# Performance work log

Hardware: AMD Instinct MI355X
Metric: run time of the kernel (lower is better)

## Reference

```python
import jax, jax.numpy as jnp
import numpy as np

B, S, D, H, F, V = 64, 64, 512, 8, 2048, 8192
L = 6
ENC_C = 2048  # InceptionV3 feature channels
NEG_INF = jnp.float32(-jnp.inf)


def _layernorm(x, g, b, eps=1e-3):
    mu = jnp.mean(x, axis=-1, keepdims=True)
    var = jnp.var(x, axis=-1, keepdims=True)
    return (x - mu) * jax.lax.rsqrt(var + eps) * g + b


def _mha(q_in, kv_in, Wq, Wk, Wv, Wo, causal=False):
    Bq, Sq, Dm = q_in.shape
    Sk = kv_in.shape[1]
    dh = Dm // H
    q = (q_in @ Wq).reshape(Bq, Sq, H, dh)
    k = (kv_in @ Wk).reshape(Bq, Sk, H, dh)
    v = (kv_in @ Wv).reshape(Bq, Sk, H, dh)
    scores = jnp.einsum('bqhd,bkhd->bhqk', q, k) / jnp.sqrt(jnp.float32(dh))
    if causal:
        mask = jnp.tril(jnp.ones((Sq, Sk), dtype=bool))
        scores = jnp.where(mask, scores, jnp.float32(-1e9))
    a = jax.nn.softmax(scores, axis=-1)
    o = jnp.einsum('bhqk,bkhd->bqhd', a, v).reshape(Bq, Sq, Dm)
    return o @ Wo


def replacement_mask(targets):
    # out[b,i,v] = -inf iff some j<=i has targets[b,j]==v and v!=0
    valid = (targets != 0)[..., None].astype(jnp.float32)  # (B,S,1)
    oh = jax.nn.one_hot(targets, V, dtype=jnp.float32) * valid  # (B,S,V)
    seen = jnp.cumsum(oh, axis=1) > 0
    return jnp.where(seen, NEG_INF, jnp.float32(0.0))


def setup_inputs() -> dict:
    key = jax.random.key(0)
    ks = jax.random.split(key, 32)
    n = lambda i, shp, sc=0.02: jax.random.normal(ks[i], shp, jnp.float32) * sc
    inp = {
        'enc_feat': jax.random.normal(ks[0], (B, 8, 8, ENC_C), jnp.float32),
        'targets': jax.random.randint(ks[1], (B, S), 0, V, jnp.int32),
        'conv_w': n(2, (ENC_C, D)), 'conv_b': jnp.zeros((D,), jnp.float32),
        'tok_emb': n(3, (V, D)), 'pos_emb': n(4, (S, D)),
        'Wq_s': n(5, (L, D, D)), 'Wk_s': n(6, (L, D, D)),
        'Wv_s': n(7, (L, D, D)), 'Wo_s': n(8, (L, D, D)),
        'Wq_c': n(9, (L, D, D)), 'Wk_c': n(10, (L, D, D)),
        'Wv_c': n(11, (L, D, D)), 'Wo_c': n(12, (L, D, D)),
        'W1': n(13, (L, D, F)), 'fb1': jnp.zeros((L, F), jnp.float32),
        'W2': n(14, (L, F, D)), 'fb2': jnp.zeros((L, D), jnp.float32),
        'g1': jnp.ones((L, D), jnp.float32), 'be1': jnp.zeros((L, D), jnp.float32),
        'g2': jnp.ones((L, D), jnp.float32), 'be2': jnp.zeros((L, D), jnp.float32),
        'g3': jnp.ones((L, D), jnp.float32), 'be3': jnp.zeros((L, D), jnp.float32),
        'Wout': n(15, (D, V)), 'bout': jnp.zeros((V,), jnp.float32),
    }
    return inp


def reference(enc_feat, conv_w, conv_b, tok_emb, pos_emb,
              Wq_s, Wk_s, Wv_s, Wo_s, Wq_c, Wk_c, Wv_c, Wo_c,
              W1, fb1, W2, fb2, g1, be1, g2, be2, g3, be3,
              Wout, bout, targets):
    # 1x1 conv == per-pixel matmul, then flatten spatial -> (B, 64, D)
    enc = enc_feat.reshape(B, -1, ENC_C) @ conv_w + conv_b
    # decoder: token + positional embedding
    x = tok_emb[targets] + pos_emb[None, :, :]
    for l in range(L):
        a1 = _mha(x, x, Wq_s[l], Wk_s[l], Wv_s[l], Wo_s[l], causal=True)
        x = _layernorm(x + a1, g1[l], be1[l])
        a2 = _mha(x, enc, Wq_c[l], Wk_c[l], Wv_c[l], Wo_c[l])
        x = _layernorm(x + a2, g2[l], be2[l])
        ff = jax.nn.relu(x @ W1[l] + fb1[l]) @ W2[l] + fb2[l]
        x = _layernorm(x + ff, g3[l], be3[l])
    logits = x @ Wout + bout
    return logits + replacement_mask(targets)
```

## Files before the change

kernel.cpp:

```cpp
#include <hip/hip_runtime.h>
#include <cstdint>
#include <cstddef>

#define SS   64
#define BB   64
#define DM   512
#define NH   8
#define DH   64
#define FF   2048
#define VV   8192
#define LL   6
#define ENCC 2048
#define MR   4096

#define MASK_SENTINEL -3.0e38f

typedef unsigned short u16;
typedef __attribute__((ext_vector_type(8))) short bf16x8;
typedef __attribute__((ext_vector_type(4))) float f32x4;

__device__ __forceinline__ u16 f2b(float f) {
    union { float f; uint32_t u; } c; c.f = f;
    uint32_t u = c.u;
    return (u16)((u + 0x7fffu + ((u >> 16) & 1u)) >> 16);
}
__device__ __forceinline__ float blo(uint32_t p) {
    union { uint32_t u; float f; } c; c.u = p << 16; return c.f;
}
__device__ __forceinline__ float bhi(uint32_t p) {
    union { uint32_t u; float f; } c; c.u = p & 0xffff0000u; return c.f;
}

#define GLL(g, l) __builtin_amdgcn_global_load_lds( \
    (const __attribute__((address_space(1))) void*)(g), \
    (__attribute__((address_space(3))) void*)(l), 16, 0, 0)

template<int BMT>
__global__ __launch_bounds__(256) void gemm_bf16(
    const u16* __restrict__ A, const u16* __restrict__ BT,
    const float* __restrict__ bias, u16* __restrict__ Cb,
    int K, int ldc, int relu, int nsplit,
    const u16* __restrict__ A2, const u16* __restrict__ BT2,
    u16* __restrict__ C2, int ldc2)
{
    constexpr int WM = BMT / 2;
    constexpr int AI = WM / 16;
    constexpr int TILE = (BMT + 128) * 32;
    __shared__ __align__(16) u16 smem[2 * TILE];
    const int tid = threadIdx.x;
    const int wave = tid >> 6, lane = tid & 63;

    int bx = blockIdx.x;
    const u16* Ab = A; const u16* Bb = BT; u16* Cp = Cb; int ld = ldc;
    const float* bi = bias; int rl = relu;
    if (bx >= nsplit) { bx -= nsplit; Ab = A2; Bb = BT2; Cp = C2; ld = ldc2; bi = nullptr; rl = 0; }

    const int m0 = blockIdx.y * BMT, n0 = bx * 128;
    const int srow = wave * 16 + (lane >> 2);
    const int scol = (lane & 3) * 8;
    const u16* Ap  = Ab + (size_t)(m0 + srow) * K + scol;
    const u16* Bp  = Bb + (size_t)(n0 + srow) * K + scol;
    const u16* Ap2 = Ap + (size_t)64 * K;
    const u16* Bp2 = Bp + (size_t)64 * K;
    const int aW = wave * 16 * 32;
    const int bW = BMT * 32 + wave * 16 * 32;

    const int wm = wave >> 1, wn = wave & 1;
    const int q = lane >> 4, mr = lane & 15;
    const int aRd = (wm * WM + mr) * 32 + q * 8;
    const int bRd = BMT * 32 + (wn * 64 + mr) * 32 + q * 8;

    f32x4 acc[AI][4];
    const f32x4 z = {0.f, 0.f, 0.f, 0.f};
#pragma unroll
    for (int i = 0; i < AI; i++)
#pragma unroll
        for (int j = 0; j < 4; j++) acc[i][j] = z;

    GLL(Ap, smem + aW);
    if constexpr (BMT == 128) GLL(Ap2, smem + aW + 64 * 32);
    GLL(Bp, smem + bW);
    GLL(Bp2, smem + bW + 64 * 32);
    Ap += 32; Ap2 += 32; Bp += 32; Bp2 += 32;
    __syncthreads();

    int cur = 0;
    for (int k0 = 0; k0 < K; k0 += 32) {
        if (k0 + 32 < K) {
            u16* nb = smem + (cur ^ 1) * TILE;
            GLL(Ap, nb + aW);
            if constexpr (BMT == 128) GLL(Ap2, nb + aW + 64 * 32);
            GLL(Bp, nb + bW);
            GLL(Bp2, nb + bW + 64 * 32);
            Ap += 32; Ap2 += 32; Bp += 32; Bp2 += 32;
        }
        const u16* cb = smem + cur * TILE;
        bf16x8 af[AI], bfr[4];
#pragma unroll
        for (int i = 0; i < AI; i++) af[i]  = *(const bf16x8*)(cb + aRd + (size_t)i * 16 * 32);
#pragma unroll
        for (int j = 0; j < 4; j++) bfr[j] = *(const bf16x8*)(cb + bRd + (size_t)j * 16 * 32);
#pragma unroll
        for (int i = 0; i < AI; i++)
#pragma unroll
            for (int j = 0; j < 4; j++)
                acc[i][j] = __builtin_amdgcn_mfma_f32_16x16x32_bf16(af[i], bfr[j], acc[i][j], 0, 0, 0);
        __syncthreads();
        cur ^= 1;
    }

    float* ep = (float*)smem + wave * 1024;
    const int lq = lane >> 4, lmr = lane & 15;
    const int colb = n0 + wn * 64 + lmr * 4;
    float4 b4 = make_float4(0.f, 0.f, 0.f, 0.f);
    if (bi) b4 = *(const float4*)(bi + colb);
#pragma unroll
    for (int i = 0; i < AI; i++) {
#pragma unroll
        for (int j = 0; j < 4; j++)
#pragma unroll
            for (int r = 0; r < 4; r++)
                ep[(q * 4 + r) * 64 + j * 16 + mr] = acc[i][j][r];
        __syncthreads();
#pragma unroll
        for (int p = 0; p < 4; p++) {
            const int lr = p * 4 + lq;
            float4 v = *(const float4*)(ep + lr * 64 + lmr * 4);
            v.x += b4.x; v.y += b4.y; v.z += b4.z; v.w += b4.w;
            if (rl) {
                v.x = fmaxf(v.x, 0.f); v.y = fmaxf(v.y, 0.f);
                v.z = fmaxf(v.z, 0.f); v.w = fmaxf(v.w, 0.f);
            }
            uint2 pk;
            pk.x = (uint32_t)f2b(v.x) | ((uint32_t)f2b(v.y) << 16);
            pk.y = (uint32_t)f2b(v.z) | ((uint32_t)f2b(v.w) << 16);
            const int row = m0 + wm * WM + i * 16 + lr;
            *(uint2*)(Cp + (size_t)row * ld + colb) = pk;
        }
        __syncthreads();
    }
}

__global__ __launch_bounds__(256) void gemm_logits_mfma(
    const u16* __restrict__ A, const u16* __restrict__ BT,
    const float* __restrict__ bias, const int* __restrict__ fo,
    float* __restrict__ C, int K)
{
    constexpr int TILE = 256 * 32;
    __shared__ __align__(16) u16 smem[2 * TILE];
    const int tid = threadIdx.x;
    const int wave = tid >> 6, lane = tid & 63;
    const int m0 = blockIdx.y * 128, n0 = blockIdx.x * 128;

    const int srow = wave * 16 + (lane >> 2);
    const int scol = (lane & 3) * 8;
    const u16* Ap  = A  + (size_t)(m0 + srow) * K + scol;
    const u16* Bp  = BT + (size_t)(n0 + srow) * K + scol;
    const u16* Ap2 = Ap + (size_t)64 * K;
    const u16* Bp2 = Bp + (size_t)64 * K;
    const int aW = wave * 16 * 32;
    const int bW = 128 * 32 + wave * 16 * 32;

    const int wm = wave >> 1, wn = wave & 1;
    const int q = lane >> 4, mr = lane & 15;
    const int aRd = (wm * 64 + mr) * 32 + q * 8;
    const int bRd = 128 * 32 + (wn * 64 + mr) * 32 + q * 8;

    f32x4 acc[4][4];
    const f32x4 z = {0.f, 0.f, 0.f, 0.f};
#pragma unroll
    for (int i = 0; i < 4; i++)
#pragma unroll
        for (int j = 0; j < 4; j++) acc[i][j] = z;

    GLL(Ap,  smem + aW);
    GLL(Ap2, smem + aW + 64 * 32);
    GLL(Bp,  smem + bW);
    GLL(Bp2, smem + bW + 64 * 32);
    Ap += 32; Ap2 += 32; Bp += 32; Bp2 += 32;
    __syncthreads();

    int cur = 0;
    for (int k0 = 0; k0 < K; k0 += 32) {
        if (k0 + 32 < K) {
            u16* nb = smem + (cur ^ 1) * TILE;
            GLL(Ap,  nb + aW);
            GLL(Ap2, nb + aW + 64 * 32);
            GLL(Bp,  nb + bW);
            GLL(Bp2, nb + bW + 64 * 32);
            Ap += 32; Ap2 += 32; Bp += 32; Bp2 += 32;
        }
        const u16* cb = smem + cur * TILE;
        bf16x8 af[4], bfr[4];
#pragma unroll
        for (int i = 0; i < 4; i++) af[i]  = *(const bf16x8*)(cb + aRd + (size_t)i * 16 * 32);
#pragma unroll
        for (int j = 0; j < 4; j++) bfr[j] = *(const bf16x8*)(cb + bRd + (size_t)j * 16 * 32);
#pragma unroll
        for (int i = 0; i < 4; i++)
#pragma unroll
            for (int j = 0; j < 4; j++)
                acc[i][j] = __builtin_amdgcn_mfma_f32_16x16x32_bf16(af[i], bfr[j], acc[i][j], 0, 0, 0);
        __syncthreads();
        cur ^= 1;
    }

    float* ep = (float*)smem + wave * 1024;
    const int lq = lane >> 4, lmr = lane & 15;
    const int colb = n0 + wn * 64 + lmr * 4;
    const float4 b4 = *(const float4*)(bias + colb);
#pragma unroll
    for (int i = 0; i < 4; i++) {
#pragma unroll
        for (int j = 0; j < 4; j++)
#pragma unroll
            for (int r = 0; r < 4; r++)
                ep[(q * 4 + r) * 64 + j * 16 + mr] = acc[i][j][r];
        __syncthreads();
#pragma unroll
        for (int p = 0; p < 4; p++) {
            const int lr = p * 4 + lq;
            const int row = m0 + wm * 64 + i * 16 + lr;
            const int b = row >> 6, pos = row & 63;
            float4 v = *(const float4*)(ep + lr * 64 + lmr * 4);
            const int4 f4 = *(const int4*)(fo + (size_t)b * VV + colb);
            v.x = (f4.x <= pos) ? MASK_SENTINEL : v.x + b4.x;
            v.y = (f4.y <= pos) ? MASK_SENTINEL : v.y + b4.y;
            v.z = (f4.z <= pos) ? MASK_SENTINEL : v.z + b4.z;
            v.w = (f4.w <= pos) ? MASK_SENTINEL : v.w + b4.w;
            *(float4*)(C + (size_t)row * VV + colb) = v;
        }
        __syncthreads();
    }
}

struct TPB {
    const float* s[8];
    u16* d[8];
    long dz[8];
};

__global__ __launch_bounds__(256) void transpose8_kernel(TPB t)
{
    __shared__ float tl[32][33];
    const int zz = blockIdx.z;
    const int m = zz / 6, l = zz - m * 6;
    const float* in = t.s[m] + (size_t)l * 262144;
    u16* out = t.d[m] + (size_t)l * t.dz[m];
    const int r0 = blockIdx.y * 32, c0 = blockIdx.x * 32;
    const int tx = threadIdx.x & 31, ty = threadIdx.x >> 5;
#pragma unroll
    for (int i = 0; i < 4; i++)
        tl[ty + 8 * i][tx] = in[(size_t)(r0 + ty + 8 * i) * 512 + c0 + tx];
    __syncthreads();
#pragma unroll
    for (int i = 0; i < 4; i++)
        out[(size_t)(c0 + ty + 8 * i) * 512 + r0 + tx] = f2b(tl[tx][ty + 8 * i]);
}

__global__ __launch_bounds__(256) void transpose_bf16_kernel(
    const float* __restrict__ in, u16* __restrict__ out,
    int R, int C, size_t in_z, size_t out_z)
{
    __shared__ float tl[32][33];
    in  += (size_t)blockIdx.z * in_z;
    out += (size_t)blockIdx.z * out_z;
    const int r0 = blockIdx.y * 32, c0 = blockIdx.x * 32;
    const int tx = threadIdx.x & 31, ty = threadIdx.x >> 5;
#pragma unroll
    for (int i = 0; i < 4; i++)
        tl[ty + 8 * i][tx] = in[(size_t)(r0 + ty + 8 * i) * C + c0 + tx];
    __syncthreads();
#pragma unroll
    for (int i = 0; i < 4; i++)
        out[(size_t)(c0 + ty + 8 * i) * R + r0 + tx] = f2b(tl[tx][ty + 8 * i]);
}

__global__ __launch_bounds__(256) void convert_bf16_kernel(
    const float* __restrict__ in, u16* __restrict__ out)
{
    const int idx = blockIdx.x * 256 + threadIdx.x;
    float4 v = *reinterpret_cast<const float4*>(in + (size_t)idx * 4);
    uint2 p;
    p.x = (uint32_t)f2b(v.x) | ((uint32_t)f2b(v.y) << 16);
    p.y = (uint32_t)f2b(v.z) | ((uint32_t)f2b(v.w) << 16);
    *reinterpret_cast<uint2*>(out + (size_t)idx * 4) = p;
}

__global__ __launch_bounds__(256) void attn_kernel(
    const u16* __restrict__ qg, int qld,
    const u16* __restrict__ kg, const u16* __restrict__ vg, int kvld,
    u16* __restrict__ og, int causal)
{
    __shared__ float qs[SS][68];
    __shared__ float ks[SS][68];
    __shared__ float vs[SS][68];
    __shared__ float red[SS][8];
    float (*ps)[68] = qs;

    const int tid = threadIdx.x;
    const int bh = blockIdx.x;
    const int b = bh >> 3, h = bh & 7;
    const size_t qbase = (size_t)b * SS * qld + (size_t)h * DH;
    const size_t kbase = (size_t)b * SS * kvld + (size_t)h * DH;
    const size_t obase = (size_t)b * SS * DM + (size_t)h * DH;

#pragma unroll
    for (int it = 0; it < 4; it++) {
        int idx = tid + 256 * it;
        int s = idx >> 4;
        int d4 = (idx & 15) << 2;
        uint2 a = *(const uint2*)(qg + qbase + (size_t)s * qld + d4);
        qs[s][d4 + 0] = blo(a.x); qs[s][d4 + 1] = bhi(a.x);
        qs[s][d4 + 2] = blo(a.y); qs[s][d4 + 3] = bhi(a.y);
        uint2 c = *(const uint2*)(kg + kbase + (size_t)s * kvld + d4);
        ks[s][d4 + 0] = blo(c.x); ks[s][d4 + 1] = bhi(c.x);
        ks[s][d4 + 2] = blo(c.y); ks[s][d4 + 3] = bhi(c.y);
        uint2 e = *(const uint2*)(vg + kbase + (size_t)s * kvld + d4);
        vs[s][d4 + 0] = blo(e.x); vs[s][d4 + 1] = bhi(e.x);
        vs[s][d4 + 2] = blo(e.y); vs[s][d4 + 3] = bhi(e.y);
    }
    __syncthreads();

    const int r = tid >> 2, c = tid & 3;

    float sc[16];
#pragma unroll
    for (int jj = 0; jj < 16; jj++) sc[jj] = 0.f;
    for (int d4 = 0; d4 < 64; d4 += 4) {
        float4 qv = *reinterpret_cast<const float4*>(&qs[r][d4]);
#pragma unroll
        for (int jj = 0; jj < 16; jj++) {
            int j = jj * 4 + c;
            float4 kv = *reinterpret_cast<const float4*>(&ks[j][d4]);
            sc[jj] += qv.x * kv.x + qv.y * kv.y + qv.z * kv.z + qv.w * kv.w;
        }
    }
    float mx = -1e30f;
#pragma unroll
    for (int jj = 0; jj < 16; jj++) {
        int j = jj * 4 + c;
        float s_ = sc[jj] * 0.125f;
        if (causal && j > r) s_ = -1e9f;
        sc[jj] = s_;
        mx = fmaxf(mx, s_);
    }
    red[r][c] = mx;
    __syncthreads();
    float m = fmaxf(fmaxf(red[r][0], red[r][1]), fmaxf(red[r][2], red[r][3]));
    float sum = 0.f;
#pragma unroll
    for (int jj = 0; jj < 16; jj++) {
        float p = expf(sc[jj] - m);
        sc[jj] = p;
        sum += p;
    }
    red[r][4 + c] = sum;
    __syncthreads();
    float tot = red[r][4] + red[r][5] + red[r][6] + red[r][7];
    float inv = 1.f / tot;
#pragma unroll
    for (int jj = 0; jj < 16; jj++) ps[r][jj * 4 + c] = sc[jj] * inv;
    __syncthreads();

    float acc[16];
#pragma unroll
    for (int i = 0; i < 16; i++) acc[i] = 0.f;
    for (int j = 0; j < 64; j++) {
        float pj = ps[r][j];
#pragma unroll
        for (int dd = 0; dd < 4; dd++) {
            float4 vv = *reinterpret_cast<const float4*>(&vs[j][c * 16 + dd * 4]);
            acc[dd * 4 + 0] += pj * vv.x;
            acc[dd * 4 + 1] += pj * vv.y;
            acc[dd * 4 + 2] += pj * vv.z;
            acc[dd * 4 + 3] += pj * vv.w;
        }
    }
#pragma unroll
    for (int dd = 0; dd < 4; dd++) {
        uint2 p;
        p.x = (uint32_t)f2b(acc[dd * 4 + 0]) | ((uint32_t)f2b(acc[dd * 4 + 1]) << 16);
        p.y = (uint32_t)f2b(acc[dd * 4 + 2]) | ((uint32_t)f2b(acc[dd * 4 + 3]) << 16);
        *reinterpret_cast<uint2*>(&og[obase + (size_t)r * DM + c * 16 + dd * 4]) = p;
    }
}

__global__ __launch_bounds__(256) void add_ln_kernel(
    const float* __restrict__ x, const u16* __restrict__ a,
    const float* __restrict__ g, const float* __restrict__ be,
    float* __restrict__ y, u16* __restrict__ yb)
{
    const int wave = threadIdx.x >> 6, lane = threadIdx.x & 63;
    const int row = blockIdx.x * 4 + wave;
    const float* xr = x + (size_t)row * DM;
    const u16* ar = a + (size_t)row * DM;
    float* yr = y + (size_t)row * DM;
    u16* ybr = yb + (size_t)row * DM;

    float vbuf[8];
    float sum = 0.f, sq = 0.f;
#pragma unroll
    for (int i = 0; i < 2; i++) {
        int d = lane * 8 + i * 4;
        float4 xv = *reinterpret_cast<const float4*>(&xr[d]);
        uint2 av = *(const uint2*)(ar + d);
        float a0 = blo(av.x), a1 = bhi(av.x), a2 = blo(av.y), a3 = bhi(av.y);
        float v0 = xv.x + a0, v1 = xv.y + a1, v2 = xv.z + a2, v3 = xv.w + a3;
        vbuf[i * 4 + 0] = v0; vbuf[i * 4 + 1] = v1;
        vbuf[i * 4 + 2] = v2; vbuf[i * 4 + 3] = v3;
        sum += v0 + v1 + v2 + v3;
        sq += v0 * v0 + v1 * v1 + v2 * v2 + v3 * v3;
    }
#pragma unroll
    for (int off = 32; off; off >>= 1) {
        sum += __shfl_xor(sum, off, 64);
        sq  += __shfl_xor(sq, off, 64);
    }
    float mean = sum * (1.f / 512.f);
    float var = sq * (1.f / 512.f) - mean * mean;
    float rs = rsqrtf(var + 1e-3f);
#pragma unroll
    for (int i = 0; i < 2; i++) {
        int d = lane * 8 + i * 4;
        float4 gv = *reinterpret_cast<const float4*>(&g[d]);
        float4 bv = *reinterpret_cast<const float4*>(&be[d]);
        float4 ov;
        ov.x = (vbuf[i * 4 + 0] - mean) * rs * gv.x + bv.x;
        ov.y = (vbuf[i * 4 + 1] - mean) * rs * gv.y + bv.y;
        ov.z = (vbuf[i * 4 + 2] - mean) * rs * gv.z + bv.z;
        ov.w = (vbuf[i * 4 + 3] - mean) * rs * gv.w + bv.w;
        *reinterpret_cast<float4*>(&yr[d]) = ov;
        uint2 p;
        p.x = (uint32_t)f2b(ov.x) | ((uint32_t)f2b(ov.y) << 16);
        p.y = (uint32_t)f2b(ov.z) | ((uint32_t)f2b(ov.w) << 16);
        *reinterpret_cast<uint2*>(&ybr[d]) = p;
    }
}

__global__ __launch_bounds__(256) void embed_kernel(
    const int* __restrict__ targets, const float* __restrict__ tok,
    const float* __restrict__ pos, float* __restrict__ x, u16* __restrict__ xb)
{
    int idx = blockIdx.x * 256 + threadIdx.x;
    int row = idx >> 7;
    int d4 = (idx & 127) << 2;
    int s = row & 63;
    int t = targets[row];
    float4 tv = *reinterpret_cast<const float4*>(&tok[(size_t)t * DM + d4]);
    float4 pv = *reinterpret_cast<const float4*>(&pos[(size_t)s * DM + d4]);
    float4 ov = make_float4(tv.x + pv.x, tv.y + pv.y, tv.z + pv.z, tv.w + pv.w);
    *reinterpret_cast<float4*>(&x[(size_t)row * DM + d4]) = ov;
    uint2 p;
    p.x = (uint32_t)f2b(ov.x) | ((uint32_t)f2b(ov.y) << 16);
    p.y = (uint32_t)f2b(ov.z) | ((uint32_t)f2b(ov.w) << 16);
    *reinterpret_cast<uint2*>(&xb[(size_t)row * DM + d4]) = p;
}

__global__ __launch_bounds__(256) void init_fo_kernel(int* __restrict__ fo)
{
    fo[blockIdx.x * 256 + threadIdx.x] = SS;
}

__global__ __launch_bounds__(256) void scatter_fo_kernel(
    const int* __restrict__ targets, int* __restrict__ fo)
{
    int i = blockIdx.x * 256 + threadIdx.x;
    int t = targets[i];
    if (t != 0) atomicMin(&fo[(size_t)(i >> 6) * VV + t], i & 63);
}

extern "C" void kernel_launch(void* const* d_in, const int* in_sizes, int n_in,
                              void* d_out, int out_size, void* d_ws, size_t ws_size,
                              hipStream_t stream)
{
    const float* enc_feat = (const float*)d_in[0];
    const int*   targets  = (const int*)d_in[1];
    const float* conv_w   = (const float*)d_in[2];
    const float* conv_b   = (const float*)d_in[3];
    const float* tok_emb  = (const float*)d_in[4];
    const float* pos_emb  = (const float*)d_in[5];
    const float* Wq_s     = (const float*)d_in[6];
    const float* Wk_s     = (const float*)d_in[7];
    const float* Wv_s     = (const float*)d_in[8];
    const float* Wo_s     = (const float*)d_in[9];
    const float* Wq_c     = (const float*)d_in[10];
    const float* Wk_c     = (const float*)d_in[11];
    const float* Wv_c     = (const float*)d_in[12];
    const float* Wo_c     = (const float*)d_in[13];
    const float* W1       = (const float*)d_in[14];
    const float* fb1      = (const float*)d_in[15];
    const float* W2       = (const float*)d_in[16];
    const float* fb2      = (const float*)d_in[17];
    const float* g1       = (const float*)d_in[18];
    const float* be1      = (const float*)d_in[19];
    const float* g2       = (const float*)d_in[20];
    const float* be2      = (const float*)d_in[21];
    const float* g3       = (const float*)d_in[22];
    const float* be3      = (const float*)d_in[23];
    const float* Wout     = (const float*)d_in[24];
    const float* bout     = (const float*)d_in[25];
    float* out = (float*)d_out;

    u16* base = (u16*)d_ws;
    float* x   = (float*)d_ws;
    u16* xb    = base + 4194304;
    u16* projb = base + 6291456;
    u16* qcb   = base + 8388608;
    u16* attnb = base + 10485760;
    u16* encb  = base + 12582912;
    u16* big   = base + 14680064;
    int* fo    = (int*)(base + 23068672);
    u16* qkvT  = base + 24117248;
    u16* woTs  = base + 28835840;
    u16* wqTc  = base + 30408704;
    u16* kvTc  = base + 31981568;
    u16* woTc  = base + 35127296;
    u16* w1T   = base + 36700160;
    u16* w2T   = base + 42991616;
    u16* cvT   = base + 49283072;
    u16* woutT = base + 50331648;
    u16* kvAll = base + 54525952;

    const dim3 blk(256);

    init_fo_kernel<<<dim3(BB * VV / 256), blk, 0, stream>>>(fo);
    scatter_fo_kernel<<<dim3(MR / 256), blk, 0, stream>>>(targets, fo);
    embed_kernel<<<dim3(MR * DM / 4 / 256), blk, 0, stream>>>(targets, tok_emb, pos_emb, x, xb);
    convert_bf16_kernel<<<dim3(MR * ENCC / 4 / 256), blk, 0, stream>>>(enc_feat, big);

    TPB tp;
    tp.s[0] = Wq_s; tp.d[0] = qkvT;          tp.dz[0] = 786432;
    tp.s[1] = Wk_s; tp.d[1] = qkvT + 262144; tp.dz[1] = 786432;
    tp.s[2] = Wv_s; tp.d[2] = qkvT + 524288; tp.dz[2] = 786432;
    tp.s[3] = Wo_s; tp.d[3] = woTs;          tp.dz[3] = 262144;
    tp.s[4] = Wq_c; tp.d[4] = wqTc;          tp.dz[4] = 262144;
    tp.s[5] = Wk_c; tp.d[5] = kvTc;          tp.dz[5] = 524288;
    tp.s[6] = Wv_c; tp.d[6] = kvTc + 262144; tp.dz[6] = 524288;
    tp.s[7] = Wo_c; tp.d[7] = woTc;          tp.dz[7] = 262144;
    transpose8_kernel<<<dim3(16, 16, 48), blk, 0, stream>>>(tp);
    transpose_bf16_kernel<<<dim3(64, 16, 6), blk, 0, stream>>>(W1, w1T, 512, 2048, 1048576, 1048576);
    transpose_bf16_kernel<<<dim3(16, 64, 6), blk, 0, stream>>>(W2, w2T, 2048, 512, 1048576, 1048576);
    transpose_bf16_kernel<<<dim3(16, 64, 1), blk, 0, stream>>>(conv_w, cvT, 2048, 512, 0, 0);
    transpose_bf16_kernel<<<dim3(256, 16, 1), blk, 0, stream>>>(Wout, woutT, 512, 8192, 0, 0);

    gemm_bf16<64><<<dim3(4, 64), blk, 0, stream>>>(big, cvT, conv_b, encb, ENCC, DM, 0, 9999,
                                                   nullptr, nullptr, nullptr, 0);

    gemm_bf16<128><<<dim3(48, 32), blk, 0, stream>>>(encb, kvTc, nullptr, kvAll, DM, 6144, 0, 9999,
                                                     nullptr, nullptr, nullptr, 0);

    for (int l = 0; l < LL; l++) {
        gemm_bf16<128><<<dim3(12, 32), blk, 0, stream>>>(xb, qkvT + (size_t)l * 786432, nullptr,
                                                         big, DM, 1536, 0, 9999,
                                                         nullptr, nullptr, nullptr, 0);
        attn_kernel<<<dim3(BB * NH), blk, 0, stream>>>(big, 1536, big + 512, big + 1024, 1536, attnb, 1);
        gemm_bf16<64><<<dim3(4, 64), blk, 0, stream>>>(attnb, woTs + (size_t)l * 262144, nullptr,
                                                       projb, DM, DM, 0, 9999,
                                                       nullptr, nullptr, nullptr, 0);
        add_ln_kernel<<<dim3(MR / 4), blk, 0, stream>>>(x, projb, g1 + l * DM, be1 + l * DM, x, xb);
        gemm_bf16<64><<<dim3(4, 64), blk, 0, stream>>>(xb, wqTc + (size_t)l * 262144, nullptr,
                                                       qcb, DM, DM, 0, 9999,
                                                       nullptr, nullptr, nullptr, 0);
        attn_kernel<<<dim3(BB * NH), blk, 0, stream>>>(qcb, 512,
                                                       kvAll + (size_t)l * 1024,
                                                       kvAll + (size_t)l * 1024 + 512, 6144, attnb, 0);
        gemm_bf16<64><<<dim3(4, 64), blk, 0, stream>>>(attnb, woTc + (size_t)l * 262144, nullptr,
                                                       projb, DM, DM, 0, 9999,
                                                       nullptr, nullptr, nullptr, 0);
        add_ln_kernel<<<dim3(MR / 4), blk, 0, stream>>>(x, projb, g2 + l * DM, be2 + l * DM, x, xb);
        gemm_bf16<128><<<dim3(16, 32), blk, 0, stream>>>(xb, w1T + (size_t)l * 1048576,
                                                         fb1 + (size_t)l * FF, big, DM, FF, 1, 9999,
                                                         nullptr, nullptr, nullptr, 0);
        gemm_bf16<64><<<dim3(4, 64), blk, 0, stream>>>(big, w2T + (size_t)l * 1048576,
                                                       fb2 + (size_t)l * DM, projb, FF, DM, 0, 9999,
                                                       nullptr, nullptr, nullptr, 0);
        add_ln_kernel<<<dim3(MR / 4), blk, 0, stream>>>(x, projb, g3 + l * DM, be3 + l * DM, x, xb);
    }

    gemm_logits_mfma<<<dim3(64, 32), blk, 0, stream>>>(xb, woutT, bout, fo, out, DM);
}
```

Measured before the change: 1.331 ms.

## Triple-buffer GEMM K-loop with vmcnt waits and use smaller tiles for more blocks

Replaces the double-buffered LDS pipeline in both GEMM kernels with a three-stage ring. Prefetches are issued two steps ahead, and partial vmcnt waits plus a raw s_barrier replace the per-iteration __syncthreads. The generic GEMM also gains a BN template parameter, and most launches move to 64x64 or 64x128 tiles so the small M=4096 GEMMs spread over more workgroups. This trades more LDS per block and a heavier per-tile overhead for better latency hiding and more CU coverage.

```diff
diff --git a/kernel.cpp b/kernel.cpp
--- a/kernel.cpp
+++ b/kernel.cpp
@@ -35,37 +35,42 @@
     (const __attribute__((address_space(1))) void*)(g), \
     (__attribute__((address_space(3))) void*)(l), 16, 0, 0)
 
-template<int BMT>
+#define WAITV2 asm volatile("s_waitcnt vmcnt(2)" ::: "memory")
+#define WAITV3 asm volatile("s_waitcnt vmcnt(3)" ::: "memory")
+#define WAITV4 asm volatile("s_waitcnt vmcnt(4)" ::: "memory")
+#define WAITV0 asm volatile("s_waitcnt vmcnt(0)" ::: "memory")
+#define WAITL0 asm volatile("s_waitcnt lgkmcnt(0)" ::: "memory")
+
+template<int BMT, int BNT>
 __global__ __launch_bounds__(256) void gemm_bf16(
     const u16* __restrict__ A, const u16* __restrict__ BT,
     const float* __restrict__ bias, u16* __restrict__ Cb,
-    int K, int ldc, int relu, int nsplit,
-    const u16* __restrict__ A2, const u16* __restrict__ BT2,
-    u16* __restrict__ C2, int ldc2)
-{
-    constexpr int WM = BMT / 2;
+    int K, int ldc, int relu)
+{
+    constexpr int WNW = (BNT == 128) ? 2 : 1;
+    constexpr int WMW = 4 / WNW;
+    constexpr int WM = BMT / WMW;
     constexpr int AI = WM / 16;
-    constexpr int TILE = (BMT + 128) * 32;
-    __shared__ __align__(16) u16 smem[2 * TILE];
+    constexpr int AG = BMT / 64;
+    constexpr int BG = BNT / 64;
+    constexpr int G  = AG + BG;
+    constexpr int TILE = (BMT + BNT) * 32;
+    __shared__ __align__(16) u16 smem[3 * TILE];
     const int tid = threadIdx.x;
     const int wave = tid >> 6, lane = tid & 63;
 
-    int bx = blockIdx.x;
-    const u16* Ab = A; const u16* Bb = BT; u16* Cp = Cb; int ld = ldc;
-    const float* bi = bias; int rl = relu;
-    if (bx >= nsplit) { bx -= nsplit; Ab = A2; Bb = BT2; Cp = C2; ld = ldc2; bi = nullptr; rl = 0; }
-
-    const int m0 = blockIdx.y * BMT, n0 = bx * 128;
+    const int m0 = blockIdx.y * BMT, n0 = blockIdx.x * BNT;
     const int srow = wave * 16 + (lane >> 2);
     const int scol = (lane & 3) * 8;
-    const u16* Ap  = Ab + (size_t)(m0 + srow) * K + scol;
-    const u16* Bp  = Bb + (size_t)(n0 + srow) * K + scol;
+    const u16* Ap  = A  + (size_t)(m0 + srow) * K + scol;
+    const u16* Bp  = BT + (size_t)(n0 + srow) * K + scol;
     const u16* Ap2 = Ap + (size_t)64 * K;
     const u16* Bp2 = Bp + (size_t)64 * K;
     const int aW = wave * 16 * 32;
     const int bW = BMT * 32 + wave * 16 * 32;
 
-    const int wm = wave >> 1, wn = wave & 1;
+    const int wm = (BNT == 128) ? (wave >> 1) : wave;
+    const int wn = (BNT == 128) ? (wave & 1) : 0;
     const int q = lane >> 4, mr = lane & 15;
     const int aRd = (wm * WM + mr) * 32 + q * 8;
     const int bRd = BMT * 32 + (wn * 64 + mr) * 32 + q * 8;
@@ -77,43 +82,65 @@
 #pragma unroll
         for (int j = 0; j < 4; j++) acc[i][j] = z;
 
-    GLL(Ap, smem + aW);
-    if constexpr (BMT == 128) GLL(Ap2, smem + aW + 64 * 32);
-    GLL(Bp, smem + bW);
-    GLL(Bp2, smem + bW + 64 * 32);
-    Ap += 32; Ap2 += 32; Bp += 32; Bp2 += 32;
-    __syncthreads();
-
-    int cur = 0;
-    for (int k0 = 0; k0 < K; k0 += 32) {
-        if (k0 + 32 < K) {
-            u16* nb = smem + (cur ^ 1) * TILE;
-            GLL(Ap, nb + aW);
-            if constexpr (BMT == 128) GLL(Ap2, nb + aW + 64 * 32);
-            GLL(Bp, nb + bW);
-            GLL(Bp2, nb + bW + 64 * 32);
-            Ap += 32; Ap2 += 32; Bp += 32; Bp2 += 32;
-        }
-        const u16* cb = smem + cur * TILE;
+#define STAGE(buf) do { \
+        GLL(Ap, (buf) + aW); \
+        if constexpr (AG == 2) GLL(Ap2, (buf) + aW + 64 * 32); \
+        GLL(Bp, (buf) + bW); \
+        if constexpr (BG == 2) GLL(Bp2, (buf) + bW + 64 * 32); \
+        Ap += 32; Bp += 32; \
+        if constexpr (AG == 2) Ap2 += 32; \
+        if constexpr (BG == 2) Bp2 += 32; \
+    } while (0)
+
+    u16* rd = smem;
+    u16* md = smem + TILE;
+    u16* pf = smem + 2 * TILE;
+    STAGE(rd);
+    STAGE(md);
+    const int NS = K >> 5;
+
+    for (int k = 0; k < NS - 1; k++) {
+        if constexpr (G == 2) WAITV2;
+        else if constexpr (G == 3) WAITV3;
+        else WAITV4;
+        __builtin_amdgcn_s_barrier();
         bf16x8 af[AI], bfr[4];
 #pragma unroll
-        for (int i = 0; i < AI; i++) af[i]  = *(const bf16x8*)(cb + aRd + (size_t)i * 16 * 32);
-#pragma unroll
-        for (int j = 0; j < 4; j++) bfr[j] = *(const bf16x8*)(cb + bRd + (size_t)j * 16 * 32);
+        for (int i = 0; i < AI; i++) af[i]  = *(const bf16x8*)(rd + aRd + i * 16 * 32);
+#pragma unroll
+        for (int j = 0; j < 4; j++) bfr[j] = *(const bf16x8*)(rd + bRd + j * 16 * 32);
+        WAITL0;
+        __builtin_amdgcn_sched_barrier(0);
+        if (k + 2 < NS) STAGE(pf);
 #pragma unroll
         for (int i = 0; i < AI; i++)
 #pragma unroll
             for (int j = 0; j < 4; j++)
                 acc[i][j] = __builtin_amdgcn_mfma_f32_16x16x32_bf16(af[i], bfr[j], acc[i][j], 0, 0, 0);
-        __syncthreads();
-        cur ^= 1;
-    }
+        u16* t = rd; rd = md; md = pf; pf = t;
+    }
+    WAITV0;
+    __builtin_amdgcn_s_barrier();
+    {
+        bf16x8 af[AI], bfr[4];
+#pragma unroll
+        for (int i = 0; i < AI; i++) af[i]  = *(const bf16x8*)(rd + aRd + i * 16 * 32);
+#pragma unroll
+        for (int j = 0; j < 4; j++) bfr[j] = *(const bf16x8*)(rd + bRd + j * 16 * 32);
+#pragma unroll
+        for (int i = 0; i < AI; i++)
+#pragma unroll
+            for (int j = 0; j < 4; j++)
+                acc[i][j] = __builtin_amdgcn_mfma_f32_16x16x32_bf16(af[i], bfr[j], acc[i][j], 0, 0, 0);
+    }
+    __syncthreads();
+#undef STAGE
 
     float* ep = (float*)smem + wave * 1024;
     const int lq = lane >> 4, lmr = lane & 15;
     const int colb = n0 + wn * 64 + lmr * 4;
     float4 b4 = make_float4(0.f, 0.f, 0.f, 0.f);
-    if (bi) b4 = *(const float4*)(bi + colb);
+    if (bias) b4 = *(const float4*)(bias + colb);
 #pragma unroll
     for (int i = 0; i < AI; i++) {
 #pragma unroll
@@ -127,7 +154,7 @@
             const int lr = p * 4 + lq;
             float4 v = *(const float4*)(ep + lr * 64 + lmr * 4);
             v.x += b4.x; v.y += b4.y; v.z += b4.z; v.w += b4.w;
-            if (rl) {
+            if (relu) {
                 v.x = fmaxf(v.x, 0.f); v.y = fmaxf(v.y, 0.f);
                 v.z = fmaxf(v.z, 0.f); v.w = fmaxf(v.w, 0.f);
             }
@@ -135,7 +162,7 @@
             pk.x = (uint32_t)f2b(v.x) | ((uint32_t)f2b(v.y) << 16);
             pk.y = (uint32_t)f2b(v.z) | ((uint32_t)f2b(v.w) << 16);
             const int row = m0 + wm * WM + i * 16 + lr;
-            *(uint2*)(Cp + (size_t)row * ld + colb) = pk;
+            *(uint2*)(Cb + (size_t)row * ldc + colb) = pk;
         }
         __syncthreads();
     }
@@ -147,7 +174,7 @@
     float* __restrict__ C, int K)
 {
     constexpr int TILE = 256 * 32;
-    __shared__ __align__(16) u16 smem[2 * TILE];
+    __shared__ __align__(16) u16 smem[3 * TILE];
     const int tid = threadIdx.x;
     const int wave = tid >> 6, lane = tid & 63;
     const int m0 = blockIdx.y * 128, n0 = blockIdx.x * 128;
@@ -173,37 +200,55 @@
 #pragma unroll
         for (int j = 0; j < 4; j++) acc[i][j] = z;
 
-    GLL(Ap,  smem + aW);
-    GLL(Ap2, smem + aW + 64 * 32);
-    GLL(Bp,  smem + bW);
-    GLL(Bp2, smem + bW + 64 * 32);
-    Ap += 32; Ap2 += 32; Bp += 32; Bp2 += 32;
-    __syncthreads();
-
-    int cur = 0;
-    for (int k0 = 0; k0 < K; k0 += 32) {
-        if (k0 + 32 < K) {
-            u16* nb = smem + (cur ^ 1) * TILE;
-            GLL(Ap,  nb + aW);
-            GLL(Ap2, nb + aW + 64 * 32);
-            GLL(Bp,  nb + bW);
-            GLL(Bp2, nb + bW + 64 * 32);
-            Ap += 32; Ap2 += 32; Bp += 32; Bp2 += 32;
-        }
-        const u16* cb = smem + cur * TILE;
+#define STAGE4(buf) do { \
+        GLL(Ap,  (buf) + aW); \
+        GLL(Ap2, (buf) + aW + 64 * 32); \
+        GLL(Bp,  (buf) + bW); \
+        GLL(Bp2, (buf) + bW + 64 * 32); \
+        Ap += 32; Ap2 += 32; Bp += 32; Bp2 += 32; \
+    } while (0)
+
+    u16* rd = smem;
+    u16* md = smem + TILE;
+    u16* pf = smem + 2 * TILE;
+    STAGE4(rd);
+    STAGE4(md);
+    const int NS = K >> 5;
+
+    for (int k = 0; k < NS - 1; k++) {
+        WAITV4;
+        __builtin_amdgcn_s_barrier();
         bf16x8 af[4], bfr[4];
 #pragma unroll
-        for (int i = 0; i < 4; i++) af[i]  = *(const bf16x8*)(cb + aRd + (size_t)i * 16 * 32);
-#pragma unroll
-        for (int j = 0; j < 4; j++) bfr[j] = *(const bf16x8*)(cb + bRd + (size_t)j * 16 * 32);
+        for (int i = 0; i < 4; i++) af[i]  = *(const bf16x8*)(rd + aRd + i * 16 * 32);
+#pragma unroll
+        for (int j = 0; j < 4; j++) bfr[j] = *(const bf16x8*)(rd + bRd + j * 16 * 32);
+        WAITL0;
+        __builtin_amdgcn_sched_barrier(0);
+        if (k + 2 < NS) STAGE4(pf);
 #pragma unroll
         for (int i = 0; i < 4; i++)
 #pragma unroll
             for (int j = 0; j < 4; j++)
                 acc[i][j] = __builtin_amdgcn_mfma_f32_16x16x32_bf16(af[i], bfr[j], acc[i][j], 0, 0, 0);
-        __syncthreads();
-        cur ^= 1;
-    }
+        u16* t = rd; rd = md; md = pf; pf = t;
+    }
+    WAITV0;
+    __builtin_amdgcn_s_barrier();
+    {
+        bf16x8 af[4], bfr[4];
+#pragma unroll
+        for (int i = 0; i < 4; i++) af[i]  = *(const bf16x8*)(rd + aRd + i * 16 * 32);
+#pragma unroll
+        for (int j = 0; j < 4; j++) bfr[j] = *(const bf16x8*)(rd + bRd + j * 16 * 32);
+#pragma unroll
+        for (int i = 0; i < 4; i++)
+#pragma unroll
+            for (int j = 0; j < 4; j++)
+                acc[i][j] = __builtin_amdgcn_mfma_f32_16x16x32_bf16(af[i], bfr[j], acc[i][j], 0, 0, 0);
+    }
+    __syncthreads();
+#undef STAGE4
 
     float* ep = (float*)smem + wave * 1024;
     const int lq = lane >> 4, lmr = lane & 15;
@@ -544,37 +589,29 @@
     transpose_bf16_kernel<<<dim3(16, 64, 1), blk, 0, stream>>>(conv_w, cvT, 2048, 512, 0, 0);
     transpose_bf16_kernel<<<dim3(256, 16, 1), blk, 0, stream>>>(Wout, woutT, 512, 8192, 0, 0);
 
-    gemm_bf16<64><<<dim3(4, 64), blk, 0, stream>>>(big, cvT, conv_b, encb, ENCC, DM, 0, 9999,
-                                                   nullptr, nullptr, nullptr, 0);
-
-    gemm_bf16<128><<<dim3(48, 32), blk, 0, stream>>>(encb, kvTc, nullptr, kvAll, DM, 6144, 0, 9999,
-                                                     nullptr, nullptr, nullptr, 0);
+    gemm_bf16<64, 64><<<dim3(8, 64), blk, 0, stream>>>(big, cvT, conv_b, encb, ENCC, DM, 0);
+
+    gemm_bf16<64, 128><<<dim3(48, 64), blk, 0, stream>>>(encb, kvTc, nullptr, kvAll, DM, 6144, 0);
 
     for (int l = 0; l < LL; l++) {
-        gemm_bf16<128><<<dim3(12, 32), blk, 0, stream>>>(xb, qkvT + (size_t)l * 786432, nullptr,
-                                                         big, DM, 1536, 0, 9999,
-                                                         nullptr, nullptr, nullptr, 0);
+        gemm_bf16<64, 128><<<dim3(12, 64), blk, 0, stream>>>(xb, qkvT + (size_t)l * 786432, nullptr,
+                                                             big, DM, 1536, 0);
         attn_kernel<<<dim3(BB * NH), blk, 0, stream>>>(big, 1536, big + 512, big + 1024, 1536, attnb, 1);
-        gemm_bf16<64><<<dim3(4, 64), blk, 0, stream>>>(attnb, woTs + (size_t)l * 262144, nullptr,
-                                                       projb, DM, DM, 0, 9999,
-                                                       nullptr, nullptr, nullptr, 0);
+        gemm_bf16<64, 64><<<dim3(8, 64), blk, 0, stream>>>(attnb, woTs + (size_t)l * 262144, nullptr,
+                                                           projb, DM, DM, 0);
         add_ln_kernel<<<dim3(MR / 4), blk, 0, stream>>>(x, projb, g1 + l * DM, be1 + l * DM, x, xb);
-        gemm_bf16<64><<<dim3(4, 64), blk, 0, stream>>>(xb, wqTc + (size_t)l * 262144, nullptr,
-                                                       qcb, DM, DM, 0, 9999,
-                                                       nullptr, nullptr, nullptr, 0);
+        gemm_bf16<64, 64><<<dim3(8, 64), blk, 0, stream>>>(xb, wqTc + (size_t)l * 262144, nullptr,
+                                                           qcb, DM, DM, 0);
         attn_kernel<<<dim3(BB * NH), blk, 0, stream>>>(qcb, 512,
                                                        kvAll + (size_t)l * 1024,
                                                        kvAll + (size_t)l * 1024 + 512, 6144, attnb, 0);
-        gemm_bf16<64><<<dim3(4, 64), blk, 0, stream>>>(attnb, woTc + (size_t)l * 262144, nullptr,
-                                                       projb, DM, DM, 0, 9999,
-                                                       nullptr, nullptr, nullptr, 0);
+        gemm_bf16<64, 64><<<dim3(8, 64), blk, 0, stream>>>(attnb, woTc + (size_t)l * 262144, nullptr,
+                                                           projb, DM, DM, 0);
         add_ln_kernel<<<dim3(MR / 4), blk, 0, stream>>>(x, projb, g2 + l * DM, be2 + l * DM, x, xb);
-        gemm_bf16<128><<<dim3(16, 32), blk, 0, stream>>>(xb, w1T + (size_t)l * 1048576,
-                                                         fb1 + (size_t)l * FF, big, DM, FF, 1, 9999,
-                                                         nullptr, nullptr, nullptr, 0);
-        gemm_bf16<64><<<dim3(4, 64), blk, 0, stream>>>(big, w2T + (size_t)l * 1048576,
-                                                       fb2 + (size_t)l * DM, projb, FF, DM, 0, 9999,
-                                                       nullptr, nullptr, nullptr, 0);
+        gemm_bf16<64, 128><<<dim3(16, 64), blk, 0, stream>>>(xb, w1T + (size_t)l * 1048576,
+                                                             fb1 + (size_t)l * FF, big, DM, FF, 1);
+        gemm_bf16<64, 64><<<dim3(8, 64), blk, 0, stream>>>(big, w2T + (size_t)l * 1048576,
+                                                           fb2 + (size_t)l * DM, projb, FF, DM, 0);
         add_ln_kernel<<<dim3(MR / 4), blk, 0, stream>>>(x, projb, g3 + l * DM, be3 + l * DM, x, xb);
     }
 
```

New measurement: 1.240 ms. 6.9% less time.
